# Optimization experiments

Measured on AMD Instinct MI355X. Metric: run time of the kernel, lower is better.

## Reference

```python
import jax, jax.numpy as jnp
import numpy as np

N, E, ET = 100000, 1000000, 200000
F, D, H, L = 64, 32, 66, 2
BN_EPS = 1e-5

def _w(key, shape):
    fan_in = shape[-2] if len(shape) >= 2 else shape[-1]
    return jax.random.normal(key, shape, dtype=jnp.float32) / np.sqrt(fan_in)

def setup_inputs() -> dict:
    key = jax.random.key(0)
    ks = jax.random.split(key, 30)
    inp = {
        'x': jax.random.normal(ks[0], (N, F), dtype=jnp.float32),
        'edge_index': jax.random.randint(ks[1], (2, E), 0, N),
        'edge_attr': jax.random.normal(ks[2], (E, D), dtype=jnp.float32),
        'edge_label_index': jax.random.randint(ks[3], (2, ET), 0, N),
        'target_edge_attr': jax.random.normal(ks[4], (ET, D), dtype=jnp.float32),
        # embeddings
        'node_w': _w(ks[5], (F, H)), 'node_b': jnp.zeros((H,), jnp.float32),
        'edge_w': _w(ks[6], (D, H)), 'edge_b': jnp.zeros((H,), jnp.float32),
        # per-layer GINEConv MLP (Linear-ReLU-Linear), stacked over layers
        'conv_w1': _w(ks[7], (L, H, H)), 'conv_b1': jnp.zeros((L, H), jnp.float32),
        'conv_w2': _w(ks[8], (L, H, H)), 'conv_b2': jnp.zeros((L, H), jnp.float32),
        # per-layer BatchNorm affine params
        'bn_gamma': jnp.ones((L, H), jnp.float32), 'bn_beta': jnp.zeros((L, H), jnp.float32),
        # per-layer edge-update MLP (3H -> H -> H)
        'emlp_w1': _w(ks[9], (L, 3 * H, H)), 'emlp_b1': jnp.zeros((L, H), jnp.float32),
        'emlp_w2': _w(ks[10], (L, H, H)), 'emlp_b2': jnp.zeros((L, H), jnp.float32),
        # final classifier MLP (3H -> 50 -> 25 -> 2); dropout treated as eval (identity)
        'mlp_w1': _w(ks[11], (3 * H, 50)), 'mlp_b1': jnp.zeros((50,), jnp.float32),
        'mlp_w2': _w(ks[12], (50, 25)), 'mlp_b2': jnp.zeros((25,), jnp.float32),
        'mlp_w3': _w(ks[13], (25, 2)), 'mlp_b3': jnp.zeros((2,), jnp.float32),
    }
    return inp

def reference(x, edge_attr, target_edge_attr, node_w, node_b, edge_w, edge_b,
              conv_w1, conv_b1, conv_w2, conv_b2, bn_gamma, bn_beta,
              emlp_w1, emlp_b1, emlp_w2, emlp_b2,
              mlp_w1, mlp_b1, mlp_w2, mlp_b2, mlp_w3, mlp_b3,
              edge_index, edge_label_index):
    n = x.shape[0]
    src, dst = edge_index[0], edge_index[1]
    tsrc, tdst = edge_label_index[0], edge_label_index[1]
    h = x @ node_w + node_b              # [N, H]
    ea = edge_attr @ edge_w + edge_b     # [E, H]
    tea = target_edge_attr @ edge_w + edge_b  # [ET, H]
    n_layers = conv_w1.shape[0]
    for i in range(n_layers):
        # GINEConv: (1+eps)*x + sum_j relu(x_j + e_ij), eps=0, then MLP
        msg = jax.nn.relu(h[src] + ea)                               # [E, H]
        aggr = jax.ops.segment_sum(msg, dst, num_segments=n)         # [N, H]
        z = h + aggr
        z = jax.nn.relu(z @ conv_w1[i] + conv_b1[i]) @ conv_w2[i] + conv_b2[i]
        # BatchNorm (training-mode batch stats, biased variance)
        mean = z.mean(axis=0)
        var = jnp.var(z, axis=0)
        z = (z - mean) * jax.lax.rsqrt(var + BN_EPS) * bn_gamma[i] + bn_beta[i]
        h = (h + jax.nn.relu(z)) / 2
        # edge update on target edges
        cat = jnp.concatenate([h[tsrc], h[tdst], tea], axis=-1)      # [ET, 3H]
        upd = jax.nn.relu(cat @ emlp_w1[i] + emlp_b1[i]) @ emlp_w2[i] + emlp_b2[i]
        tea = tea + upd / 2
    pair = jax.nn.relu(jnp.concatenate([h[tsrc], h[tdst]], axis=-1))  # [ET, 2H]
    feat = jnp.concatenate([pair, tea], axis=-1)                      # [ET, 3H]
    o = jax.nn.relu(feat @ mlp_w1 + mlp_b1)
    o = jax.nn.relu(o @ mlp_w2 + mlp_b2)
    return o @ mlp_w3 + mlp_b3
```

## Files before the change

kernel.cpp:

```cpp
#include <hip/hip_runtime.h>

#define NN 100000
#define NE 1000000
#define NT 200000
#define SCB 391

typedef __attribute__((ext_vector_type(8))) short short8;
typedef __attribute__((ext_vector_type(4))) float f32x4;

__device__ __forceinline__ unsigned short f2b(float x) {
  union { float f; unsigned int u; } v; v.f = x;
  unsigned int r = v.u + 0x7fffu + ((v.u >> 16) & 1u);
  return (unsigned short)(r >> 16);
}
__device__ __forceinline__ float b2f(unsigned short x) {
  union { unsigned int u; float f; } v; v.u = ((unsigned int)x) << 16;
  return v.f;
}

struct PrepTab {
  const float* a[14]; const float* b[14];
  int K[14], C[14], rows[14], off[14];
};

__global__ __launch_bounds__(256) void prep_w(PrepTab tab, unsigned short* wT) {
  int s = blockIdx.x;
  const float* A = tab.a[s];
  const float* B = tab.b[s];
  int K = tab.K[s], C = tab.C[s], rows = tab.rows[s];
  unsigned short* dst = wT + tab.off[s];
  int n = rows * 104;
  for (int i = threadIdx.x; i < n; i += 256) {
    int c = i / 104, k = i - c * 104;
    float v = 0.0f;
    if (k < K) {
      if (c < C) v = A[k * C + c];
      else if (B && c < 2 * C) v = B[k * C + (c - C)];
    }
    dst[i] = f2b(v);
  }
}

template<int K, int KSTEPS, int CT, int C, int AIN, int ROUT>
__global__ __launch_bounds__(256) void mfma_gemm(
    const void* __restrict__ in, const float* __restrict__ add,
    const unsigned short* __restrict__ Bt, const float* __restrict__ bias,
    void* __restrict__ outp, void* __restrict__ out2, int R)
{
  constexpr int CR = CT * 16;
  __shared__ __align__(16) unsigned short As[64 * 104];
  __shared__ __align__(16) unsigned short Bs[CR * 104];
  __shared__ float bs[CR];
  const int t = threadIdx.x;
  const int r0 = blockIdx.x * 64;
  for (int i = t; i < CT * 208; i += 256) ((uint4*)Bs)[i] = ((const uint4*)Bt)[i];
  if (t < CR) bs[t] = (bias && t < C) ? bias[t] : 0.0f;
  constexpr int KH = KSTEPS * 16;
  for (int i = t; i < 64 * KH; i += 256) {
    int r = i / KH, kk = (i - r * KH) * 2;
    int rg = r0 + r;
    unsigned short u0 = 0, u1 = 0;
    if (rg < R && kk < K) {
      if constexpr (AIN == 3) {
        unsigned int u = ((const unsigned int*)in)[((size_t)rg * K + kk) >> 1];
        u0 = u & 0xffffu; u1 = u >> 16;
      } else {
        float2 f = *(const float2*)((const float*)in + (size_t)rg * K + kk);
        float v0 = f.x, v1 = f.y;
        if constexpr (AIN == 1) {
          float2 g = *(const float2*)(add + (size_t)rg * K + kk);
          v0 += g.x; v1 += g.y;
        }
        if constexpr (AIN == 2) { v0 = fmaxf(v0, 0.f); v1 = fmaxf(v1, 0.f); }
        u0 = f2b(v0); u1 = f2b(v1);
      }
    }
    As[r * 104 + kk] = u0; As[r * 104 + kk + 1] = u1;
  }
  __syncthreads();
  const int lane = t & 63, w = t >> 6, m = lane & 15, q = lane >> 4;
  f32x4 acc[CT] = {};
  const unsigned short* Ap = As + (w * 16 + m) * 104 + q * 8;
  const unsigned short* Bp = Bs + m * 104 + q * 8;
#pragma unroll
  for (int ks = 0; ks < KSTEPS; ks++) {
    short8 a = *(const short8*)(Ap + ks * 32);
#pragma unroll
    for (int ct = 0; ct < CT; ct++) {
      short8 b = *(const short8*)(Bp + ct * 16 * 104 + ks * 32);
      acc[ct] = __builtin_amdgcn_mfma_f32_16x16x32_bf16(a, b, acc[ct], 0, 0, 0);
    }
  }
#pragma unroll
  for (int ct = 0; ct < CT; ct++) {
    int c = ct * 16 + m;
    if (c < C) {
      float bv = bs[c];
#pragma unroll
      for (int r2 = 0; r2 < 4; r2++) {
        int row = r0 + w * 16 + q * 4 + r2;
        if (row < R) {
          float v = acc[ct][r2] + bv;
          if constexpr ((ROUT & 1) != 0) v = fmaxf(v, 0.f);
          if constexpr ((ROUT & 2) != 0)
            ((unsigned short*)outp)[(size_t)row * C + c] = f2b(v);
          else
            ((float*)outp)[(size_t)row * C + c] = v;
          if constexpr ((ROUT & 4) != 0)
            ((unsigned short*)out2)[(size_t)row * C + c] = f2b(v);
        }
      }
    }
  }
}

__global__ __launch_bounds__(256) void hist_kernel(const int* __restrict__ ei,
                                                   int* __restrict__ deg)
{
  int e = blockIdx.x * 256 + threadIdx.x;
  if (e < NE) atomicAdd(&deg[ei[NE + e]], 1);
}

__global__ __launch_bounds__(256) void blocksum_k(const int* __restrict__ deg,
                                                  int* __restrict__ bsum)
{
  __shared__ int red[256];
  const int t = threadIdx.x;
  int i = blockIdx.x * 256 + t;
  red[t] = (i < NN) ? deg[i] : 0;
  __syncthreads();
  for (int s = 128; s > 0; s >>= 1) {
    if (t < s) red[t] += red[t + s];
    __syncthreads();
  }
  if (t == 0) bsum[blockIdx.x] = red[0];
}

__global__ __launch_bounds__(512) void scansums_k(int* __restrict__ bsum,
                                                  int* __restrict__ rowptr)
{
  __shared__ int s[512];
  const int t = threadIdx.x;
  s[t] = (t < SCB) ? bsum[t] : 0;
  __syncthreads();
  for (int off = 1; off < 512; off <<= 1) {
    int v = (t >= off) ? s[t - off] : 0;
    __syncthreads();
    s[t] += v;
    __syncthreads();
  }
  if (t < SCB) bsum[t] = (t == 0) ? 0 : s[t - 1];
  if (t == 0) rowptr[NN] = NE;
}

__global__ __launch_bounds__(256) void scatter_scan_k(
    const int* __restrict__ deg, const int* __restrict__ bsum,
    int* __restrict__ rowptr)
{
  __shared__ int s[256];
  const int t = threadIdx.x;
  int i = blockIdx.x * 256 + t;
  int v = (i < NN) ? deg[i] : 0;
  s[t] = v;
  __syncthreads();
  for (int off = 1; off < 256; off <<= 1) {
    int x = (t >= off) ? s[t - off] : 0;
    __syncthreads();
    s[t] += x;
    __syncthreads();
  }
  if (i < NN) rowptr[i] = bsum[blockIdx.x] + s[t] - v;
}

__global__ __launch_bounds__(256) void fill_kernel(
    const int* __restrict__ ei, const int* __restrict__ rowptr,
    int* __restrict__ cur, int* __restrict__ srcS, int* __restrict__ dstS,
    int* __restrict__ permS, int* __restrict__ invp)
{
  int e = blockIdx.x * 256 + threadIdx.x;
  if (e >= NE) return;
  int d = ei[NE + e];
  int pos = atomicAdd(&cur[d], 1);
  int w = rowptr[d] + pos;
  srcS[w] = ei[e];
  dstS[w] = d;
  permS[w] = e;
  invp[e] = w;
}

__global__ __launch_bounds__(256) void perm_eattr(
    const float* __restrict__ eattr, const int* __restrict__ invp,
    unsigned short* __restrict__ eaB)
{
  int i = blockIdx.x * 256 + threadIdx.x;
  if (i >= NE * 16) return;
  int e = i >> 4, j = i & 15;
  float2 f = ((const float2*)eattr)[i];
  unsigned int packed = (unsigned int)f2b(f.x) | ((unsigned int)f2b(f.y) << 16);
  ((unsigned int*)eaB)[(size_t)invp[e] * 16 + j] = packed;
}

__global__ __launch_bounds__(256) void eaw_kernel(
    const unsigned short* __restrict__ eaB, const float* __restrict__ eattr,
    const int* __restrict__ permS, const unsigned short* __restrict__ Bt,
    const float* __restrict__ bias, unsigned short* __restrict__ eaW)
{
  __shared__ __align__(16) unsigned short As[64 * 40];
  __shared__ __align__(16) unsigned short Bs[80 * 104];
  __shared__ float bs[80];
  const int t = threadIdx.x;
  const int e0 = blockIdx.x * 64;
  for (int i = t; i < 1040; i += 256) ((uint4*)Bs)[i] = ((const uint4*)Bt)[i];
  if (t < 80) bs[t] = (t < 66) ? bias[t] : 0.0f;
  if (eaB) {
    for (int i = t; i < 1024; i += 256) {
      int r = i >> 4, j = i & 15;
      unsigned int u = ((const unsigned int*)eaB)[(size_t)(e0 + r) * 16 + j];
      As[r * 40 + j * 2] = u & 0xffffu;
      As[r * 40 + j * 2 + 1] = u >> 16;
    }
  } else {
    for (int i = t; i < 1024; i += 256) {
      int r = i >> 4, j = i & 15;
      int p = permS[e0 + r];
      float2 f = ((const float2*)(eattr + (size_t)p * 32))[j];
      As[r * 40 + j * 2] = f2b(f.x);
      As[r * 40 + j * 2 + 1] = f2b(f.y);
    }
  }
  __syncthreads();
  const int lane = t & 63, w = t >> 6, m = lane & 15, q = lane >> 4;
  f32x4 acc[5] = {};
  short8 a = *(const short8*)(As + (w * 16 + m) * 40 + q * 8);
#pragma unroll
  for (int ct = 0; ct < 5; ct++) {
    short8 b = *(const short8*)(Bs + (ct * 16 + m) * 104 + q * 8);
    acc[ct] = __builtin_amdgcn_mfma_f32_16x16x32_bf16(a, b, acc[ct], 0, 0, 0);
  }
#pragma unroll
  for (int ct = 0; ct < 5; ct++) {
    int c = ct * 16 + m;
    if (c < 66) {
      float bv = bs[c];
#pragma unroll
      for (int r2 = 0; r2 < 4; r2++) {
        int e = w * 16 + q * 4 + r2;
        eaW[(size_t)(e0 + e) * 66 + c] = f2b(acc[ct][r2] + bv);
      }
    }
  }
}

__global__ __launch_bounds__(256) void msg_aggr3(
    const int* __restrict__ rowptr, const int* __restrict__ srcS,
    const int* __restrict__ dstS, const unsigned int* __restrict__ eaW32,
    const unsigned int* __restrict__ hB32, float* __restrict__ aggr)
{
  __shared__ float msgS[64 * 67];
  __shared__ int sidx[64], didx[64];
  __shared__ int runStart[65];
  __shared__ int nrunsS;
  const int t = threadIdx.x;
  const int e0 = blockIdx.x * 64;
  if (t < 64) { sidx[t] = srcS[e0 + t]; didx[t] = dstS[e0 + t]; }
  __syncthreads();
  if (t < 64) {
    bool b = (t == 0) || (didx[t] != didx[t - 1]);
    unsigned long long mask = __ballot(b);
    int idx = __popcll(mask & ((1ull << t) - 1ull));
    if (b) runStart[idx] = t;
    if (t == 63) { nrunsS = __popcll(mask); runStart[__popcll(mask)] = 64; }
  }
  for (int idx = t; idx < 64 * 33; idx += 256) {
    int e = idx / 33, j = idx - e * 33;
    unsigned int ua = eaW32[(size_t)e0 * 33 + idx];
    unsigned int uh = hB32[(size_t)sidx[e] * 33 + j];
    float v0 = b2f((unsigned short)(ua & 0xffffu)) + b2f((unsigned short)(uh & 0xffffu));
    float v1 = b2f((unsigned short)(ua >> 16)) + b2f((unsigned short)(uh >> 16));
    msgS[e * 67 + 2 * j]     = fmaxf(v0, 0.f);
    msgS[e * 67 + 2 * j + 1] = fmaxf(v1, 0.f);
  }
  __syncthreads();
  const int nr = nrunsS;
  for (int task = t; task < nr * 66; task += 256) {
    int r = task / 66, c = task - r * 66;
    int s0 = runStart[r], s1 = runStart[r + 1];
    float s = 0.0f;
    for (int e = s0; e < s1; e++) s += msgS[e * 67 + c];
    int n = didx[s0];
    bool partial = false;
    if (r == 0)      partial = (rowptr[n] < e0);
    if (r == nr - 1) partial = partial || (rowptr[n + 1] > e0 + 64);
    if (partial) atomicAdd(&aggr[(size_t)n * 66 + c], s);
    else         aggr[(size_t)n * 66 + c] = s;
  }
}

__global__ __launch_bounds__(256) void msg_aggr2(
    const int* __restrict__ rowptr, const int* __restrict__ srcS,
    const int* __restrict__ dstS, const unsigned short* __restrict__ eaB,
    const float* __restrict__ eattr, const int* __restrict__ permS,
    const unsigned short* __restrict__ Bt, const float* __restrict__ bias,
    const unsigned short* __restrict__ hB, float* __restrict__ aggr)
{
  __shared__ __align__(16) unsigned short As[64 * 40];
  __shared__ __align__(16) unsigned short Bs[80 * 104];
  __shared__ float msgS[64 * 67];
  __shared__ float bs[80];
  __shared__ int sidx[64], didx[64];
  __shared__ int runStart[65];
  __shared__ int nrunsS;
  const int t = threadIdx.x;
  const int e0 = blockIdx.x * 64;
  for (int i = t; i < 1040; i += 256) ((uint4*)Bs)[i] = ((const uint4*)Bt)[i];
  if (t < 80) bs[t] = (t < 66) ? bias[t] : 0.0f;
  if (t < 64) { sidx[t] = srcS[e0 + t]; didx[t] = dstS[e0 + t]; }
  if (eaB) {
    for (int i = t; i < 1024; i += 256) {
      int r = i >> 4, j = i & 15;
      unsigned int u = ((const unsigned int*)eaB)[(size_t)(e0 + r) * 16 + j];
      As[r * 40 + j * 2] = u & 0xffffu;
      As[r * 40 + j * 2 + 1] = u >> 16;
    }
  } else {
    for (int i = t; i < 1024; i += 256) {
      int r = i >> 4, j = i & 15;
      int p = permS[e0 + r];
      float2 f = ((const float2*)(eattr + (size_t)p * 32))[j];
      As[r * 40 + j * 2] = f2b(f.x);
      As[r * 40 + j * 2 + 1] = f2b(f.y);
    }
  }
  __syncthreads();
  if (t < 64) {
    bool b = (t == 0) || (didx[t] != didx[t - 1]);
    unsigned long long mask = __ballot(b);
    int idx = __popcll(mask & ((1ull << t) - 1ull));
    if (b) runStart[idx] = t;
    if (t == 63) { nrunsS = __popcll(mask); runStart[__popcll(mask)] = 64; }
  }
  const int lane = t & 63, w = t >> 6, m = lane & 15, q = lane >> 4;
  f32x4 acc[5] = {};
  short8 a = *(const short8*)(As + (w * 16 + m) * 40 + q * 8);
#pragma unroll
  for (int ct = 0; ct < 5; ct++) {
    short8 b = *(const short8*)(Bs + (ct * 16 + m) * 104 + q * 8);
    acc[ct] = __builtin_amdgcn_mfma_f32_16x16x32_bf16(a, b, acc[ct], 0, 0, 0);
  }
#pragma unroll
  for (int ct = 0; ct < 5; ct++) {
    int c = ct * 16 + m;
    if (c < 66) {
      float bv = bs[c];
#pragma unroll
      for (int r2 = 0; r2 < 4; r2++) {
        int e = w * 16 + q * 4 + r2;
        float v = acc[ct][r2] + bv + b2f(hB[(size_t)sidx[e] * 66 + c]);
        msgS[e * 67 + c] = fmaxf(v, 0.f);
      }
    }
  }
  __syncthreads();
  const int nr = nrunsS;
  for (int task = t; task < nr * 66; task += 256) {
    int r = task / 66, c = task - r * 66;
    int s0 = runStart[r], s1 = runStart[r + 1];
    float s = 0.0f;
    for (int e = s0; e < s1; e++) s += msgS[e * 67 + c];
    int n = didx[s0];
    bool partial = false;
    if (r == 0)      partial = (rowptr[n] < e0);
    if (r == nr - 1) partial = partial || (rowptr[n + 1] > e0 + 64);
    if (partial) atomicAdd(&aggr[(size_t)n * 66 + c], s);
    else         aggr[(size_t)n * 66 + c] = s;
  }
}

__global__ __launch_bounds__(256) void bn_stats(const float* __restrict__ z,
                                                float* __restrict__ stat)
{
  const int t = threadIdx.x;
  if (t >= 198) return;
  const int c = t % 66, rs = t / 66;
  const int r0 = blockIdx.x * 1024;
  float s1 = 0.0f, s2 = 0.0f;
  int rend = r0 + 1024; if (rend > NN) rend = NN;
  for (int r = r0 + rs; r < rend; r += 3) {
    float v = z[(size_t)r * 66 + c];
    s1 += v; s2 += v * v;
  }
  atomicAdd(&stat[c], s1);
  atomicAdd(&stat[66 + c], s2);
}

__global__ __launch_bounds__(256) void bn_update(
    float* __restrict__ h, unsigned short* __restrict__ hB,
    const float* __restrict__ z, const float* __restrict__ stat,
    const float* __restrict__ gamma, const float* __restrict__ beta)
{
  int idx = blockIdx.x * 256 + threadIdx.x;
  if (idx >= NN * 66) return;
  int c = idx % 66;
  float mean = stat[c] * (1.0f / NN);
  float var  = stat[66 + c] * (1.0f / NN) - mean * mean;
  float inv  = rsqrtf(var + 1e-5f);
  float zn   = (z[idx] - mean) * inv * gamma[c] + beta[c];
  float v = 0.5f * (h[idx] + fmaxf(zn, 0.0f));
  h[idx] = v;
  hB[idx] = f2b(v);
}

__global__ __launch_bounds__(256) void edge_fused2(
    const unsigned short* __restrict__ P12, const int* __restrict__ eli,
    const unsigned short* __restrict__ B1t, const float* __restrict__ b1,
    const unsigned short* __restrict__ B2t, const float* __restrict__ b2,
    float* __restrict__ tea)
{
  __shared__ __align__(16) unsigned short As[64 * 104];
  __shared__ __align__(16) unsigned short Bs1[80 * 104];
  __shared__ __align__(16) unsigned short Bs2[80 * 104];
  __shared__ float b1s[80], b2s[80];
  __shared__ int sidx[64], didx[64];
  const int t = threadIdx.x;
  const int e0 = blockIdx.x * 64;
  for (int i = t; i < 1040; i += 256) {
    ((uint4*)Bs1)[i] = ((const uint4*)B1t)[i];
    ((uint4*)Bs2)[i] = ((const uint4*)B2t)[i];
  }
  if (t < 80) { b1s[t] = (t < 66) ? b1[t] : 0.f; b2s[t] = (t < 66) ? b2[t] : 0.f; }
  if (t < 64) { sidx[t] = eli[e0 + t]; didx[t] = eli[NT + e0 + t]; }
  for (int i = t; i < 64 * 48; i += 256) {
    int r = i / 48, kk = (i - r * 48) * 2;
    unsigned short u0 = 0, u1 = 0;
    if (kk < 66) {
      float2 f = *(const float2*)(tea + (size_t)(e0 + r) * 66 + kk);
      u0 = f2b(f.x); u1 = f2b(f.y);
    }
    As[r * 104 + kk] = u0; As[r * 104 + kk + 1] = u1;
  }
  __syncthreads();
  const int lane = t & 63, w = t >> 6, m = lane & 15, q = lane >> 4;
  const unsigned short* Ap = As + (w * 16 + m) * 104 + q * 8;
  const unsigned short* Bp1 = Bs1 + m * 104 + q * 8;
  f32x4 acc[5] = {};
#pragma unroll
  for (int ks = 0; ks < 3; ks++) {
    short8 a = *(const short8*)(Ap + ks * 32);
#pragma unroll
    for (int ct = 0; ct < 5; ct++) {
      short8 b = *(const short8*)(Bp1 + ct * 16 * 104 + ks * 32);
      acc[ct] = __builtin_amdgcn_mfma_f32_16x16x32_bf16(a, b, acc[ct], 0, 0, 0);
    }
  }
  __syncthreads();
#pragma unroll
  for (int ct = 0; ct < 5; ct++) {
    int c = ct * 16 + m;
    if (c < 66) {
      float bv = b1s[c];
#pragma unroll
      for (int r2 = 0; r2 < 4; r2++) {
        int e = w * 16 + q * 4 + r2;
        float v = acc[ct][r2] + bv + b2f(P12[(size_t)sidx[e] * 132 + c])
                                   + b2f(P12[(size_t)didx[e] * 132 + 66 + c]);
        As[e * 104 + c] = f2b(fmaxf(v, 0.f));
      }
    }
  }
  __syncthreads();
  const unsigned short* Bp2 = Bs2 + m * 104 + q * 8;
  f32x4 acc2[5] = {};
#pragma unroll
  for (int ks = 0; ks < 3; ks++) {
    short8 a = *(const short8*)(Ap + ks * 32);
#pragma unroll
    for (int ct = 0; ct < 5; ct++) {
      short8 b = *(const short8*)(Bp2 + ct * 16 * 104 + ks * 32);
      acc2[ct] = __builtin_amdgcn_mfma_f32_16x16x32_bf16(a, b, acc2[ct], 0, 0, 0);
    }
  }
#pragma unroll
  for (int ct = 0; ct < 5; ct++) {
    int c = ct * 16 + m;
    if (c < 66) {
      float bv = b2s[c];
#pragma unroll
      for (int r2 = 0; r2 < 4; r2++) {
        int e = w * 16 + q * 4 + r2;
        size_t idx = (size_t)(e0 + e) * 66 + c;
        tea[idx] += 0.5f * (acc2[ct][r2] + bv);
      }
    }
  }
}

__global__ __launch_bounds__(256) void final_fused2(
    const float* __restrict__ tea, const unsigned short* __restrict__ P12f,
    const int* __restrict__ eli, const unsigned short* __restrict__ B1t,
    const float* __restrict__ b1, const float* __restrict__ w2,
    const float* __restrict__ b2, const float* __restrict__ w3,
    const float* __restrict__ b3, float* __restrict__ out)
{
  __shared__ __align__(16) unsigned short As[64 * 104];
  __shared__ __align__(16) unsigned short Bs[64 * 104];
  __shared__ float o1s[64 * 51];
  __shared__ float o2s[64 * 25];
  __shared__ float w2s[50 * 25], w3s[50];
  __shared__ float b1s[64], b2s[25], b3s[2];
  __shared__ int sidx[64], didx[64];
  const int t = threadIdx.x;
  const int e0 = blockIdx.x * 64;
  for (int i = t; i < 832; i += 256) ((uint4*)Bs)[i] = ((const uint4*)B1t)[i];
  for (int i = t; i < 50 * 25; i += 256) w2s[i] = w2[i];
  if (t < 50) w3s[t] = w3[t];
  if (t < 64) { b1s[t] = (t < 50) ? b1[t] : 0.f; sidx[t] = eli[e0 + t]; didx[t] = eli[NT + e0 + t]; }
  if (t < 25) b2s[t] = b2[t];
  if (t < 2)  b3s[t] = b3[t];
  for (int i = t; i < 64 * 48; i += 256) {
    int r = i / 48, kk = (i - r * 48) * 2;
    unsigned short u0 = 0, u1 = 0;
    if (kk < 66) {
      float2 f = *(const float2*)(tea + (size_t)(e0 + r) * 66 + kk);
      u0 = f2b(f.x); u1 = f2b(f.y);
    }
    As[r * 104 + kk] = u0; As[r * 104 + kk + 1] = u1;
  }
  __syncthreads();
  const int lane = t & 63, w = t >> 6, m = lane & 15, q = lane >> 4;
  const unsigned short* Ap = As + (w * 16 + m) * 104 + q * 8;
  const unsigned short* Bp = Bs + m * 104 + q * 8;
  f32x4 acc[4] = {};
#pragma unroll
  for (int ks = 0; ks < 3; ks++) {
    short8 a = *(const short8*)(Ap + ks * 32);
#pragma unroll
    for (int ct = 0; ct < 4; ct++) {
      short8 b = *(const short8*)(Bp + ct * 16 * 104 + ks * 32);
      acc[ct] = __builtin_amdgcn_mfma_f32_16x16x32_bf16(a, b, acc[ct], 0, 0, 0);
    }
  }
#pragma unroll
  for (int ct = 0; ct < 4; ct++) {
    int c = ct * 16 + m;
    if (c < 50) {
      float bv = b1s[c];
#pragma unroll
      for (int r2 = 0; r2 < 4; r2++) {
        int e = w * 16 + q * 4 + r2;
        float v = acc[ct][r2] + bv + b2f(P12f[(size_t)sidx[e] * 100 + c])
                                   + b2f(P12f[(size_t)didx[e] * 100 + 50 + c]);
        o1s[e * 51 + c] = fmaxf(v, 0.f);
      }
    }
  }
  __syncthreads();
  for (int it = t; it < 64 * 25; it += 256) {
    int e = it / 25, c = it - e * 25;
    float s = b2s[c];
    for (int k = 0; k < 50; k++) s = fmaf(o1s[e * 51 + k], w2s[k * 25 + c], s);
    o2s[e * 25 + c] = fmaxf(s, 0.f);
  }
  __syncthreads();
  if (t < 128) {
    int e = t >> 1, c = t & 1;
    float s = b3s[c];
    for (int k = 0; k < 25; k++) s = fmaf(o2s[e * 25 + k], w3s[k * 2 + c], s);
    out[(size_t)(e0 + e) * 2 + c] = s;
  }
}

extern "C" void kernel_launch(void* const* d_in, const int* in_sizes, int n_in,
                              void* d_out, int out_size, void* d_ws, size_t ws_size,
                              hipStream_t stream) {
  const float* x      = (const float*)d_in[0];
  const int*   ei     = (const int*)  d_in[1];
  const float* eattr  = (const float*)d_in[2];
  const int*   eli    = (const int*)  d_in[3];
  const float* tattr  = (const float*)d_in[4];
  const float* node_w = (const float*)d_in[5];
  const float* node_b = (const float*)d_in[6];
  const float* edge_w = (const float*)d_in[7];
  const float* edge_b = (const float*)d_in[8];
  const float* cw1    = (const float*)d_in[9];
  const float* cb1    = (const float*)d_in[10];
  const float* cw2    = (const float*)d_in[11];
  const float* cb2    = (const float*)d_in[12];
  const float* bng    = (const float*)d_in[13];
  const float* bnb    = (const float*)d_in[14];
  const float* ew1    = (const float*)d_in[15];
  const float* eb1    = (const float*)d_in[16];
  const float* ew2    = (const float*)d_in[17];
  const float* eb2    = (const float*)d_in[18];
  const float* mw1    = (const float*)d_in[19];
  const float* mb1    = (const float*)d_in[20];
  const float* mw2    = (const float*)d_in[21];
  const float* mb2    = (const float*)d_in[22];
  const float* mw3    = (const float*)d_in[23];
  const float* mb3    = (const float*)d_in[24];
  float* out = (float*)d_out;

  char* p = (char*)d_ws;
  auto alloc = [&](size_t bytes) { void* r = p; p += (bytes + 255) & ~(size_t)255; return r; };
  float* h      = (float*)alloc((size_t)NN * 66 * 4);
  unsigned short* hB = (unsigned short*)alloc((size_t)NN * 66 * 2);
  float* big    = (float*)alloc((size_t)NN * 132 * 4);
  float* zbuf   = (float*)alloc((size_t)NN * 66 * 4);
  float* tea    = (float*)alloc((size_t)NT * 66 * 4);
  float* stat   = (float*)alloc(1024);
  int*   rowptr = (int*)alloc((NN + 1) * 4);
  int*   cur    = (int*)alloc((size_t)NN * 4);
  int*   bsum   = (int*)alloc((SCB + 1) * 4);
  int*   srcS   = (int*)alloc((size_t)NE * 4);
  int*   dstS   = (int*)alloc((size_t)NE * 4);
  int*   permS  = (int*)alloc((size_t)NE * 4);
  int*   invp   = (int*)alloc((size_t)NE * 4);
  unsigned short* wT = (unsigned short*)alloc((size_t)140000 * 2);
  size_t used = (size_t)(p - (char*)d_ws);
  unsigned short* eaW = nullptr;
  if (ws_size >= used + (size_t)NE * 66 * 2 + 256)
    eaW = (unsigned short*)alloc((size_t)NE * 66 * 2);
  used = (size_t)(p - (char*)d_ws);
  unsigned short* eaB = nullptr;
  if (ws_size >= used + (size_t)NE * 32 * 2 + 256)
    eaB = (unsigned short*)alloc((size_t)NE * 32 * 2);

  const int gN = (NN + 63) / 64;
  const int gT = NT / 64;
  const int gE = NE / 64;

  hipMemsetAsync(cur, 0, (size_t)NN * sizeof(int), stream);
  hist_kernel<<<(NE + 255) / 256, 256, 0, stream>>>(ei, cur);
  blocksum_k<<<SCB, 256, 0, stream>>>(cur, bsum);
  scansums_k<<<1, 512, 0, stream>>>(bsum, rowptr);
  scatter_scan_k<<<SCB, 256, 0, stream>>>(cur, bsum, rowptr);
  hipMemsetAsync(cur, 0, (size_t)NN * sizeof(int), stream);
  fill_kernel<<<(NE + 255) / 256, 256, 0, stream>>>(ei, rowptr, cur, srcS, dstS, permS, invp);
  if (eaB)
    perm_eattr<<<(NE * 16 + 255) / 256, 256, 0, stream>>>(eattr, invp, eaB);

  PrepTab tb;
  int offs[14];
  int off = 0;
  auto set = [&](int s, const float* A, const float* B, int K, int C, int rows) {
    tb.a[s] = A; tb.b[s] = B; tb.K[s] = K; tb.C[s] = C; tb.rows[s] = rows;
    tb.off[s] = off; offs[s] = off; off += rows * 104;
  };
  set(0, node_w, nullptr, 64, 66, 80);
  set(1, edge_w, nullptr, 32, 66, 80);
  for (int l = 0; l < 2; l++) {
    set(2 + l, cw1 + (size_t)l * 4356, nullptr, 66, 66, 80);
    set(4 + l, cw2 + (size_t)l * 4356, nullptr, 66, 66, 80);
    set(6 + l, ew1 + (size_t)l * 13068 + 8712, nullptr, 66, 66, 80);
    set(8 + l, ew2 + (size_t)l * 4356, nullptr, 66, 66, 80);
    set(10 + l, ew1 + (size_t)l * 13068, ew1 + (size_t)l * 13068 + 4356,
        66, 66, 144);
  }
  set(12, mw1, mw1 + 3300, 66, 50, 112);
  set(13, mw1 + 6600, nullptr, 66, 50, 80);
  prep_w<<<14, 256, 0, stream>>>(tb, wT);

  if (eaW)
    eaw_kernel<<<gE, 256, 0, stream>>>(eaB, eattr, permS, wT + offs[1], edge_b, eaW);

  mfma_gemm<64, 2, 5, 66, 0, 4><<<gN, 256, 0, stream>>>(
      x, nullptr, wT + offs[0], node_b, h, hB, NN);
  mfma_gemm<32, 1, 5, 66, 0, 0><<<gT, 256, 0, stream>>>(
      tattr, nullptr, wT + offs[1], edge_b, tea, nullptr, NT);

  for (int l = 0; l < 2; l++) {
    hipMemsetAsync(zbuf, 0, (size_t)NN * 66 * sizeof(float), stream);
    if (eaW)
      msg_aggr3<<<gE, 256, 0, stream>>>(rowptr, srcS, dstS,
                                        (const unsigned int*)eaW,
                                        (const unsigned int*)hB, zbuf);
    else
      msg_aggr2<<<gE, 256, 0, stream>>>(rowptr, srcS, dstS, eaB, eattr, permS,
                                        wT + offs[1], edge_b, hB, zbuf);
    mfma_gemm<66, 3, 5, 66, 1, 3><<<gN, 256, 0, stream>>>(
        h, zbuf, wT + offs[2 + l], cb1 + l * 66, (unsigned short*)big, nullptr, NN);
    mfma_gemm<66, 3, 5, 66, 3, 0><<<gN, 256, 0, stream>>>(
        (unsigned short*)big, nullptr, wT + offs[4 + l], cb2 + l * 66, zbuf, nullptr, NN);
    hipMemsetAsync(stat, 0, 132 * sizeof(float), stream);
    bn_stats<<<(NN + 1023) / 1024, 256, 0, stream>>>(zbuf, stat);
    bn_update<<<(NN * 66 + 255) / 256, 256, 0, stream>>>(h, hB, zbuf, stat,
                                                         bng + l * 66, bnb + l * 66);
    mfma_gemm<66, 3, 9, 132, 0, 2><<<gN, 256, 0, stream>>>(
        h, nullptr, wT + offs[10 + l], nullptr, big, nullptr, NN);
    edge_fused2<<<gT, 256, 0, stream>>>((const unsigned short*)big, eli,
                                        wT + offs[6 + l], eb1 + l * 66,
                                        wT + offs[8 + l], eb2 + l * 66, tea);
  }

  mfma_gemm<66, 3, 7, 100, 2, 2><<<gN, 256, 0, stream>>>(
      h, nullptr, wT + offs[12], nullptr, big, nullptr, NN);
  final_fused2<<<gT, 256, 0, stream>>>(tea, (const unsigned short*)big, eli,
                                       wT + offs[13], mb1,
                                       mw2, mb2, mw3, mb3, out);
}
```

Baseline: 1.281 ms.

## Aggregate messages per destination-node block with shared-memory atomics and drop eattr permute

Replaces the edge-blocked message aggregation with a node-blocked kernel: each block owns 64 destination nodes, walks their CSR edge range, and accumulates relu(h[src]+eaW) into shared memory with LDS atomics before one plain store per node. This removes the zero-fill memset of the aggregate buffer each layer and the global atomics on block boundaries. The perm_eattr pre-permutation pass and its inverse-permutation array are also removed, so eaw_kernel now gathers fp32 edge attributes through permS directly. The tradeoffs are load imbalance across node blocks with uneven degrees, LDS atomic contention, and an uncoalesced gather in eaw_kernel.

```diff
diff --git a/kernel.cpp b/kernel.cpp
--- a/kernel.cpp
+++ b/kernel.cpp
@@ -16,6 +16,9 @@
 __device__ __forceinline__ float b2f(unsigned short x) {
   union { unsigned int u; float f; } v; v.u = ((unsigned int)x) << 16;
   return v.f;
+}
+__device__ __forceinline__ float uif(unsigned int u) {
+  union { unsigned int u; float f; } v; v.u = u; return v.f;
 }
 
 struct PrepTab {
@@ -175,7 +178,7 @@
 __global__ __launch_bounds__(256) void fill_kernel(
     const int* __restrict__ ei, const int* __restrict__ rowptr,
     int* __restrict__ cur, int* __restrict__ srcS, int* __restrict__ dstS,
-    int* __restrict__ permS, int* __restrict__ invp)
+    int* __restrict__ permS)
 {
   int e = blockIdx.x * 256 + threadIdx.x;
   if (e >= NE) return;
@@ -185,25 +188,12 @@
   srcS[w] = ei[e];
   dstS[w] = d;
   permS[w] = e;
-  invp[e] = w;
-}
-
-__global__ __launch_bounds__(256) void perm_eattr(
-    const float* __restrict__ eattr, const int* __restrict__ invp,
-    unsigned short* __restrict__ eaB)
-{
-  int i = blockIdx.x * 256 + threadIdx.x;
-  if (i >= NE * 16) return;
-  int e = i >> 4, j = i & 15;
-  float2 f = ((const float2*)eattr)[i];
-  unsigned int packed = (unsigned int)f2b(f.x) | ((unsigned int)f2b(f.y) << 16);
-  ((unsigned int*)eaB)[(size_t)invp[e] * 16 + j] = packed;
 }
 
 __global__ __launch_bounds__(256) void eaw_kernel(
-    const unsigned short* __restrict__ eaB, const float* __restrict__ eattr,
-    const int* __restrict__ permS, const unsigned short* __restrict__ Bt,
-    const float* __restrict__ bias, unsigned short* __restrict__ eaW)
+    const float* __restrict__ eattr, const int* __restrict__ permS,
+    const unsigned short* __restrict__ Bt, const float* __restrict__ bias,
+    unsigned short* __restrict__ eaW)
 {
   __shared__ __align__(16) unsigned short As[64 * 40];
   __shared__ __align__(16) unsigned short Bs[80 * 104];
@@ -212,21 +202,12 @@
   const int e0 = blockIdx.x * 64;
   for (int i = t; i < 1040; i += 256) ((uint4*)Bs)[i] = ((const uint4*)Bt)[i];
   if (t < 80) bs[t] = (t < 66) ? bias[t] : 0.0f;
-  if (eaB) {
-    for (int i = t; i < 1024; i += 256) {
-      int r = i >> 4, j = i & 15;
-      unsigned int u = ((const unsigned int*)eaB)[(size_t)(e0 + r) * 16 + j];
-      As[r * 40 + j * 2] = u & 0xffffu;
-      As[r * 40 + j * 2 + 1] = u >> 16;
-    }
-  } else {
-    for (int i = t; i < 1024; i += 256) {
-      int r = i >> 4, j = i & 15;
-      int p = permS[e0 + r];
-      float2 f = ((const float2*)(eattr + (size_t)p * 32))[j];
-      As[r * 40 + j * 2] = f2b(f.x);
-      As[r * 40 + j * 2 + 1] = f2b(f.y);
-    }
+  for (int i = t; i < 1024; i += 256) {
+    int r = i >> 4, j = i & 15;
+    int p = permS[e0 + r];
+    float2 f = ((const float2*)(eattr + (size_t)p * 32))[j];
+    As[r * 40 + j * 2] = f2b(f.x);
+    As[r * 40 + j * 2 + 1] = f2b(f.y);
   }
   __syncthreads();
   const int lane = t & 63, w = t >> 6, m = lane & 15, q = lane >> 4;
@@ -251,54 +232,65 @@
   }
 }
 
-__global__ __launch_bounds__(256) void msg_aggr3(
+__global__ __launch_bounds__(256) void node_aggr(
     const int* __restrict__ rowptr, const int* __restrict__ srcS,
     const int* __restrict__ dstS, const unsigned int* __restrict__ eaW32,
     const unsigned int* __restrict__ hB32, float* __restrict__ aggr)
 {
-  __shared__ float msgS[64 * 67];
+  __shared__ float aggrS[64 * 67];
   __shared__ int sidx[64], didx[64];
-  __shared__ int runStart[65];
-  __shared__ int nrunsS;
-  const int t = threadIdx.x;
-  const int e0 = blockIdx.x * 64;
-  if (t < 64) { sidx[t] = srcS[e0 + t]; didx[t] = dstS[e0 + t]; }
-  __syncthreads();
-  if (t < 64) {
-    bool b = (t == 0) || (didx[t] != didx[t - 1]);
-    unsigned long long mask = __ballot(b);
-    int idx = __popcll(mask & ((1ull << t) - 1ull));
-    if (b) runStart[idx] = t;
-    if (t == 63) { nrunsS = __popcll(mask); runStart[__popcll(mask)] = 64; }
-  }
-  for (int idx = t; idx < 64 * 33; idx += 256) {
-    int e = idx / 33, j = idx - e * 33;
-    unsigned int ua = eaW32[(size_t)e0 * 33 + idx];
-    unsigned int uh = hB32[(size_t)sidx[e] * 33 + j];
-    float v0 = b2f((unsigned short)(ua & 0xffffu)) + b2f((unsigned short)(uh & 0xffffu));
-    float v1 = b2f((unsigned short)(ua >> 16)) + b2f((unsigned short)(uh >> 16));
-    msgS[e * 67 + 2 * j]     = fmaxf(v0, 0.f);
-    msgS[e * 67 + 2 * j + 1] = fmaxf(v1, 0.f);
-  }
-  __syncthreads();
-  const int nr = nrunsS;
-  for (int task = t; task < nr * 66; task += 256) {
-    int r = task / 66, c = task - r * 66;
-    int s0 = runStart[r], s1 = runStart[r + 1];
-    float s = 0.0f;
-    for (int e = s0; e < s1; e++) s += msgS[e * 67 + c];
-    int n = didx[s0];
-    bool partial = false;
-    if (r == 0)      partial = (rowptr[n] < e0);
-    if (r == nr - 1) partial = partial || (rowptr[n + 1] > e0 + 64);
-    if (partial) atomicAdd(&aggr[(size_t)n * 66 + c], s);
-    else         aggr[(size_t)n * 66 + c] = s;
+  const int t = threadIdx.x;
+  const int n0 = blockIdx.x * 64;
+  const int nhi = (n0 + 64 < NN) ? (n0 + 64) : NN;
+  const int eBeg = rowptr[n0];
+  const int eEnd = rowptr[nhi];
+  for (int i = t; i < 64 * 67; i += 256) aggrS[i] = 0.0f;
+  const int el = t >> 2, q = t & 3;
+  for (int c0 = eBeg; c0 < eEnd; c0 += 64) {
+    __syncthreads();
+    if (t < 64) {
+      int e = c0 + t;
+      int ok = (e < eEnd) ? 1 : 0;
+      sidx[t] = ok ? srcS[e] : 0;
+      didx[t] = ok ? (dstS[e] - n0) : 0;
+    }
+    __syncthreads();
+    int eg = c0 + el;
+    if (eg < eEnd) {
+      const unsigned int* pe = eaW32 + (size_t)eg * 33 + q;
+      const unsigned int* ph = hB32 + (size_t)sidx[el] * 33 + q;
+      float* ar = aggrS + didx[el] * 67;
+#pragma unroll
+      for (int k = 0; k < 8; k++) {
+        unsigned int ua = __builtin_nontemporal_load(pe + 4 * k);
+        unsigned int uh = ph[4 * k];
+        int j2 = 2 * (q + 4 * k);
+        float v0 = uif(ua << 16) + uif(uh << 16);
+        float v1 = uif(ua & 0xffff0000u) + uif(uh & 0xffff0000u);
+        atomicAdd(&ar[j2],     fmaxf(v0, 0.f));
+        atomicAdd(&ar[j2 + 1], fmaxf(v1, 0.f));
+      }
+      if (q == 0) {
+        unsigned int ua = __builtin_nontemporal_load(pe + 32);
+        unsigned int uh = ph[32];
+        float v0 = uif(ua << 16) + uif(uh << 16);
+        float v1 = uif(ua & 0xffff0000u) + uif(uh & 0xffff0000u);
+        atomicAdd(&ar[64], fmaxf(v0, 0.f));
+        atomicAdd(&ar[65], fmaxf(v1, 0.f));
+      }
+    }
+  }
+  __syncthreads();
+  for (int i = t; i < 64 * 66; i += 256) {
+    int r = i / 66, c = i - r * 66;
+    int n = n0 + r;
+    if (n < NN) aggr[(size_t)n * 66 + c] = aggrS[r * 67 + c];
   }
 }
 
 __global__ __launch_bounds__(256) void msg_aggr2(
     const int* __restrict__ rowptr, const int* __restrict__ srcS,
-    const int* __restrict__ dstS, const unsigned short* __restrict__ eaB,
+    const int* __restrict__ dstS,
     const float* __restrict__ eattr, const int* __restrict__ permS,
     const unsigned short* __restrict__ Bt, const float* __restrict__ bias,
     const unsigned short* __restrict__ hB, float* __restrict__ aggr)
@@ -315,21 +307,12 @@
   for (int i = t; i < 1040; i += 256) ((uint4*)Bs)[i] = ((const uint4*)Bt)[i];
   if (t < 80) bs[t] = (t < 66) ? bias[t] : 0.0f;
   if (t < 64) { sidx[t] = srcS[e0 + t]; didx[t] = dstS[e0 + t]; }
-  if (eaB) {
-    for (int i = t; i < 1024; i += 256) {
-      int r = i >> 4, j = i & 15;
-      unsigned int u = ((const unsigned int*)eaB)[(size_t)(e0 + r) * 16 + j];
-      As[r * 40 + j * 2] = u & 0xffffu;
-      As[r * 40 + j * 2 + 1] = u >> 16;
-    }
-  } else {
-    for (int i = t; i < 1024; i += 256) {
-      int r = i >> 4, j = i & 15;
-      int p = permS[e0 + r];
-      float2 f = ((const float2*)(eattr + (size_t)p * 32))[j];
-      As[r * 40 + j * 2] = f2b(f.x);
-      As[r * 40 + j * 2 + 1] = f2b(f.y);
-    }
+  for (int i = t; i < 1024; i += 256) {
+    int r = i >> 4, j = i & 15;
+    int p = permS[e0 + r];
+    float2 f = ((const float2*)(eattr + (size_t)p * 32))[j];
+    As[r * 40 + j * 2] = f2b(f.x);
+    As[r * 40 + j * 2 + 1] = f2b(f.y);
   }
   __syncthreads();
   if (t < 64) {
@@ -613,16 +596,11 @@
   int*   srcS   = (int*)alloc((size_t)NE * 4);
   int*   dstS   = (int*)alloc((size_t)NE * 4);
   int*   permS  = (int*)alloc((size_t)NE * 4);
-  int*   invp   = (int*)alloc((size_t)NE * 4);
   unsigned short* wT = (unsigned short*)alloc((size_t)140000 * 2);
   size_t used = (size_t)(p - (char*)d_ws);
   unsigned short* eaW = nullptr;
   if (ws_size >= used + (size_t)NE * 66 * 2 + 256)
     eaW = (unsigned short*)alloc((size_t)NE * 66 * 2);
-  used = (size_t)(p - (char*)d_ws);
-  unsigned short* eaB = nullptr;
-  if (ws_size >= used + (size_t)NE * 32 * 2 + 256)
-    eaB = (unsigned short*)alloc((size_t)NE * 32 * 2);
 
   const int gN = (NN + 63) / 64;
   const int gT = NT / 64;
@@ -634,9 +612,7 @@
   scansums_k<<<1, 512, 0, stream>>>(bsum, rowptr);
   scatter_scan_k<<<SCB, 256, 0, stream>>>(cur, bsum, rowptr);
   hipMemsetAsync(cur, 0, (size_t)NN * sizeof(int), stream);
-  fill_kernel<<<(NE + 255) / 256, 256, 0, stream>>>(ei, rowptr, cur, srcS, dstS, permS, invp);
-  if (eaB)
-    perm_eattr<<<(NE * 16 + 255) / 256, 256, 0, stream>>>(eattr, invp, eaB);
+  fill_kernel<<<(NE + 255) / 256, 256, 0, stream>>>(ei, rowptr, cur, srcS, dstS, permS);
 
   PrepTab tb;
   int offs[14];
@@ -660,7 +636,7 @@
   prep_w<<<14, 256, 0, stream>>>(tb, wT);
 
   if (eaW)
-    eaw_kernel<<<gE, 256, 0, stream>>>(eaB, eattr, permS, wT + offs[1], edge_b, eaW);
+    eaw_kernel<<<gE, 256, 0, stream>>>(eattr, permS, wT + offs[1], edge_b, eaW);
 
   mfma_gemm<64, 2, 5, 66, 0, 4><<<gN, 256, 0, stream>>>(
       x, nullptr, wT + offs[0], node_b, h, hB, NN);
@@ -668,14 +644,15 @@
       tattr, nullptr, wT + offs[1], edge_b, tea, nullptr, NT);
 
   for (int l = 0; l < 2; l++) {
-    hipMemsetAsync(zbuf, 0, (size_t)NN * 66 * sizeof(float), stream);
-    if (eaW)
-      msg_aggr3<<<gE, 256, 0, stream>>>(rowptr, srcS, dstS,
+    if (eaW) {
+      node_aggr<<<gN, 256, 0, stream>>>(rowptr, srcS, dstS,
                                         (const unsigned int*)eaW,
                                         (const unsigned int*)hB, zbuf);
-    else
-      msg_aggr2<<<gE, 256, 0, stream>>>(rowptr, srcS, dstS, eaB, eattr, permS,
+    } else {
+      hipMemsetAsync(zbuf, 0, (size_t)NN * 66 * sizeof(float), stream);
+      msg_aggr2<<<gE, 256, 0, stream>>>(rowptr, srcS, dstS, eattr, permS,
                                         wT + offs[1], edge_b, hB, zbuf);
+    }
     mfma_gemm<66, 3, 5, 66, 1, 3><<<gN, 256, 0, stream>>>(
         h, zbuf, wT + offs[2 + l], cb1 + l * 66, (unsigned short*)big, nullptr, NN);
     mfma_gemm<66, 3, 5, 66, 3, 0><<<gN, 256, 0, stream>>>(
```

Result: slower. 1.883 ms (+47.0%).
